# Kernel optimization log

Measured on AMD Instinct MI355X. Metric: run time of the kernel, lower is better.

## Reference

```python
import jax, jax.numpy as jnp
import numpy as np

N = 100000   # nodes
E = 1600000  # edges (before self-loops)
IN = 128     # in_num
H1, C1 = 8, 8    # gat1: 8 heads x 8 channels -> 64 concat
OUT = 32     # out_num (gat2: 1 head x 32)


def setup_inputs() -> dict:
    key = jax.random.key(0)
    ks = jax.random.split(key, 10)
    g = lambda k, shape, fan: (jax.random.normal(k, shape, jnp.float32) / np.sqrt(fan).astype(np.float32))
    return {
        "x": jax.random.normal(ks[0], (N, IN), jnp.float32),
        "edge_index": jax.random.randint(ks[1], (2, E), 0, N, dtype=jnp.int64),
        "W1": g(ks[2], (IN, H1 * C1), IN),
        "a_src1": g(ks[3], (H1, C1), C1),
        "a_dst1": g(ks[4], (H1, C1), C1),
        "b1": jnp.zeros((H1 * C1,), jnp.float32),
        "W2": g(ks[5], (H1 * C1, OUT), H1 * C1),
        "a_src2": g(ks[6], (1, OUT), OUT),
        "a_dst2": g(ks[7], (1, OUT), OUT),
        "b2": jnp.zeros((OUT,), jnp.float32),
    }


def _gat_layer(x, src, dst, W, a_src, a_dst, b, heads, ch):
    # PyG GATConv (concat=True, negative_slope=0.2). Dropout (p=0.6) is a
    # no-op in eval mode and omitted.
    n = x.shape[0]
    h = (x @ W).reshape(n, heads, ch)                        # [N,H,C]
    al_s = jnp.einsum('nhc,hc->nh', h, a_src)                # [N,H]
    al_d = jnp.einsum('nhc,hc->nh', h, a_dst)
    e = jax.nn.leaky_relu(al_s[src] + al_d[dst], negative_slope=0.2)  # [E,H]
    # segment softmax over incoming edges of each dst node
    m = jax.lax.stop_gradient(jax.ops.segment_max(e, dst, num_segments=n))
    ex = jnp.exp(e - m[dst])
    denom = jax.ops.segment_sum(ex, dst, num_segments=n)
    alpha = ex / denom[dst]                                  # [E,H]
    out = jax.ops.segment_sum(h[src] * alpha[:, :, None], dst, num_segments=n)
    return out.reshape(n, heads * ch) + b


def reference(x, edge_index, W1, a_src1, a_dst1, b1, W2, a_src2, a_dst2, b2):
    loop = jnp.arange(N, dtype=edge_index.dtype)
    src = jnp.concatenate([edge_index[0], loop])  # add_self_loops=True (PyG default)
    dst = jnp.concatenate([edge_index[1], loop])
    h = _gat_layer(x, src, dst, W1, a_src1, a_dst1, b1, H1, C1)   # [N,64]
    out = _gat_layer(h, src, dst, W2, a_src2, a_dst2, b2, 1, OUT)  # [N,OUT]
    return out
```

## Files before the change

kernel.cpp:

```cpp
#include <hip/hip_runtime.h>
#include <hip/hip_bf16.h>


#define SLAB  4096
#define STG   8192
#define NBUCK 512

typedef float v2f __attribute__((ext_vector_type(2)));

__device__ __forceinline__ float lrelu02(float x) { return x > 0.f ? x : 0.2f * x; }

__device__ __forceinline__ unsigned short f2bf(float v) {
    __hip_bfloat16 b = __float2bfloat16(v);
    return __builtin_bit_cast(unsigned short, b);
}

__device__ __forceinline__ void accum8(uint4 hv, float ex, v2f* acc) {
    v2f ex2 = {ex, ex};
#pragma unroll
    for (int q = 0; q < 4; ++q) {
        unsigned u = (&hv.x)[q];
        v2f h2 = {__uint_as_float(u << 16), __uint_as_float(u & 0xffff0000u)};
        acc[q] = __builtin_elementwise_fma(h2, ex2, acc[q]);
    }
}

__device__ __forceinline__ v2f shfl_xor_v2(v2f v, int mask) {
    v2f r;
    r.x = __shfl_xor(v.x, mask, 64);
    r.y = __shfl_xor(v.y, mask, 64);
    return r;
}

__device__ __forceinline__ void scatter_body(char* smem, int vbid,
                                             const int* __restrict__ ei,
                                             int e_real, int e_total, unsigned M,
                                             int* __restrict__ bcur_pad,
                                             unsigned* __restrict__ pairs) {
    int* cnt   = (int*)smem;
    int* loff  = cnt + 512;
    int* lcur  = loff + 512;
    int* gbase = lcur + 512;
    int* sw    = gbase + 512;

    const int t = threadIdx.x;
    const int base = vbid * STG;
    cnt[t] = 0; cnt[t + 256] = 0;
    __syncthreads();

    int rs[STG / 256], rd[STG / 256], rb[STG / 256];
#pragma unroll
    for (int k = 0; k < STG / 256; ++k) {
        int i = base + k * 256 + t;
        bool val = i < e_total;
        int s = 0, d = 0;
        if (val) {
            if (i < e_real) { s = ei[i]; d = ei[e_real + i]; }
            else            { s = d = i - e_real; }
        }
        int b = val ? (int)__umulhi((unsigned)d, M) : -1;
        rs[k] = s; rd[k] = d; rb[k] = b;
        if (val) atomicAdd(&cnt[b], 1);
    }
    __syncthreads();

    loff[t] = cnt[t]; loff[t + 256] = cnt[t + 256];
    __syncthreads();
    for (int off = 1; off < 512; off <<= 1) {
        int v0 = (t >= off) ? loff[t - off] : 0;
        int v1 = (t + 256 >= off) ? loff[t + 256 - off] : 0;
        __syncthreads();
        loff[t] += v0; loff[t + 256] += v1;
        __syncthreads();
    }
    int e0 = loff[t] - cnt[t];
    int e1 = loff[t + 256] - cnt[t + 256];
    loff[t] = e0;           loff[t + 256] = e1;
    lcur[t] = e0;           lcur[t + 256] = e1;
    gbase[t]       = t * SLAB         + atomicAdd(&bcur_pad[t * 16], cnt[t]);
    gbase[t + 256] = (t + 256) * SLAB + atomicAdd(&bcur_pad[(t + 256) * 16],
                                                  cnt[t + 256]);
    {
        const unsigned long long Mll = M;
        cnt[t]       = (int)((((unsigned long long)t << 32) + Mll - 1) / Mll);
        cnt[t + 256] = (int)((((unsigned long long)(t + 256) << 32) + Mll - 1) / Mll);
    }
    __syncthreads();

#pragma unroll
    for (int k = 0; k < STG / 256; ++k) {
        if (rb[k] >= 0) {
            int lp = atomicAdd(&lcur[rb[k]], 1);
            sw[lp] = rs[k] | ((rd[k] - cnt[rb[k]]) << 17);
        }
    }
    __syncthreads();

#pragma unroll
    for (int q = 0; q < 2; ++q) {
        int b  = t + q * 256;
        int s0 = loff[b];
        int cb = lcur[b] - s0;
        int g  = gbase[b];
        for (int j = 0; j < cb; ++j)
            pairs[g + j] = (unsigned)sw[s0 + j];
    }
}

template<int K, int OUTC, int H, int C, int NPT, int KCHUNK>
__device__ __forceinline__ void gemm_al_body(char* smem, int vbid,
                                             const float* __restrict__ x,
                                             const float* __restrict__ W,
                                             const float* __restrict__ a_src,
                                             const float* __restrict__ a_dst,
                                             unsigned short* __restrict__ h,
                                             float* __restrict__ al_s,
                                             float* __restrict__ al_d,
                                             int n) {
    constexpr int COLG = OUTC / 4;
    constexpr int NG   = 256 / COLG;
    static_assert(NG * 8 == NPT, "tile mismatch");
    constexpr int LDX  = KCHUNK + 1;
    float* Xs = (float*)smem;
    float* Ws = Xs + NPT * LDX;

    const int t    = threadIdx.x;
    const int mg   = t / COLG;
    const int cg   = t % COLG;
    const int base = vbid * NPT;

    float acc[8][4];
#pragma unroll
    for (int i = 0; i < 8; ++i)
#pragma unroll
        for (int j = 0; j < 4; ++j) acc[i][j] = 0.f;

    for (int kc = 0; kc < K; kc += KCHUNK) {
        __syncthreads();
        constexpr int F4R = KCHUNK / 4;
        constexpr int TOTF4 = NPT * F4R;
#pragma unroll
        for (int r = 0; r < TOTF4 / 256; ++r) {
            int f4   = r * 256 + t;
            int node = f4 / F4R;
            int kq   = f4 % F4R;
            int gn   = base + node; if (gn > n - 1) gn = n - 1;
            const float4 v = *(const float4*)&x[(size_t)gn * K + kc + kq * 4];
            float* d = &Xs[node * LDX + kq * 4];
            d[0] = v.x; d[1] = v.y; d[2] = v.z; d[3] = v.w;
        }
        constexpr int WF4 = KCHUNK * OUTC / 4;
        for (int idx = t; idx < WF4; idx += 256)
            *(float4*)&Ws[idx * 4] = *(const float4*)&W[(size_t)kc * OUTC + idx * 4];
        __syncthreads();

#pragma unroll 4
        for (int k = 0; k < KCHUNK; ++k) {
            float4 b = *(const float4*)&Ws[k * OUTC + cg * 4];
            float a[8];
#pragma unroll
            for (int i = 0; i < 8; ++i) a[i] = Xs[(mg * 8 + i) * LDX + k];
#pragma unroll
            for (int i = 0; i < 8; ++i) {
                acc[i][0] += a[i] * b.x;
                acc[i][1] += a[i] * b.y;
                acc[i][2] += a[i] * b.z;
                acc[i][3] += a[i] * b.w;
            }
        }
    }

    const float4 as4 = *(const float4*)&a_src[cg * 4];
    const float4 ad4 = *(const float4*)&a_dst[cg * 4];
    constexpr int GPH = C / 4;
    const int head = cg / GPH;
#pragma unroll
    for (int i = 0; i < 8; ++i) {
        int gn = base + mg * 8 + i;
        bool ok = gn < n;
        if (ok) {
            ushort4 hv;
            hv.x = f2bf(acc[i][0]); hv.y = f2bf(acc[i][1]);
            hv.z = f2bf(acc[i][2]); hv.w = f2bf(acc[i][3]);
            *(ushort4*)&h[(size_t)gn * OUTC + cg * 4] = hv;
        }
        float ps = acc[i][0] * as4.x + acc[i][1] * as4.y +
                   acc[i][2] * as4.z + acc[i][3] * as4.w;
        float pd = acc[i][0] * ad4.x + acc[i][1] * ad4.y +
                   acc[i][2] * ad4.z + acc[i][3] * ad4.w;
#pragma unroll
        for (int s = 1; s < GPH; s <<= 1) {
            ps += __shfl_xor(ps, s, 64);
            pd += __shfl_xor(pd, s, 64);
        }
        if (ok && (cg % GPH) == 0) {
            al_s[(size_t)gn * H + head] = ps;
            al_d[(size_t)gn * H + head] = pd;
        }
    }
}

__global__ __launch_bounds__(256)
void scatter_gemm_kernel(const int* __restrict__ ei, int e_real, int e_total,
                         unsigned M, int* __restrict__ bcur_pad,
                         unsigned* __restrict__ pairs, int ns,
                         const float* __restrict__ x,
                         const float* __restrict__ W1,
                         const float* __restrict__ as1,
                         const float* __restrict__ ad1,
                         unsigned short* __restrict__ h,
                         float* __restrict__ al_s,
                         float* __restrict__ al_d, int n) {
    __shared__ __align__(16) char smem[40960];
    if ((int)blockIdx.x < ns)
        scatter_body(smem, blockIdx.x, ei, e_real, e_total, M, bcur_pad, pairs);
    else
        gemm_al_body<128, 64, 8, 8, 128, 32>(smem, blockIdx.x - ns,
                                             x, W1, as1, ad1, h, al_s, al_d, n);
}

template<int K, int OUTC, int H, int C, int NPT, int KCHUNK>
__global__ __launch_bounds__(256)
void gemm_al_kernel(const float* __restrict__ x, const float* __restrict__ W,
                    const float* __restrict__ a_src, const float* __restrict__ a_dst,
                    unsigned short* __restrict__ h, float* __restrict__ al_s,
                    float* __restrict__ al_d, int n) {
    __shared__ __align__(16) char smem[(NPT * (KCHUNK + 1) + KCHUNK * OUTC) * 4];
    gemm_al_body<K, OUTC, H, C, NPT, KCHUNK>(smem, blockIdx.x, x, W, a_src,
                                             a_dst, h, al_s, al_d, n);
}

__global__ __launch_bounds__(256)
void csr_finalize_kernel(const unsigned* __restrict__ pairs,
                         const int* __restrict__ bcur_pad,
                         unsigned M, int n,
                         int* __restrict__ offsets,
                         int* __restrict__ srcs) {
    const int b = blockIdx.x;
    const int t = threadIdx.x;
    const unsigned long long Mll = M;
    int lo = (int)((((unsigned long long)b << 32) + Mll - 1) / Mll);
    int hi = (int)((((unsigned long long)(b + 1) << 32) + Mll - 1) / Mll);
    if (lo > n) lo = n;
    if (hi > n) hi = n;
    const int R    = hi - lo;
    const int cntb = bcur_pad[b * 16];
    const unsigned* sp = pairs + (size_t)b * SLAB;

    __shared__ int bs[NBUCK];
    __shared__ int ebeg_s;
    bs[t] = bcur_pad[t * 16];
    bs[t + 256] = bcur_pad[(t + 256) * 16];
    __syncthreads();
    for (int off = 1; off < NBUCK; off <<= 1) {
        int v0 = (t >= off) ? bs[t - off] : 0;
        int v1 = (t + 256 >= off) ? bs[t + 256 - off] : 0;
        __syncthreads();
        bs[t] += v0; bs[t + 256] += v1;
        __syncthreads();
    }
    if (t == 0) ebeg_s = (b == 0) ? 0 : bs[b - 1];
    if (b == NBUCK - 1 && t == 0) offsets[n] = bs[NBUCK - 1];
    __syncthreads();
    const int ebeg = ebeg_s;

    __shared__ int deg[256], sc[256], cur[256];
    deg[t] = 0;
    __syncthreads();
    for (int j = t; j < cntb; j += 256)
        atomicAdd(&deg[sp[j] >> 17], 1);
    __syncthreads();

    sc[t] = deg[t];
    __syncthreads();
    for (int off = 1; off < 256; off <<= 1) {
        int v = (t >= off) ? sc[t - off] : 0;
        __syncthreads();
        sc[t] += v;
        __syncthreads();
    }
    int e0 = sc[t] - deg[t];
    cur[t] = e0;
    if (t < R) offsets[lo + t] = ebeg + e0;
    __syncthreads();

    for (int j = t; j < cntb; j += 256) {
        unsigned w = sp[j];
        int pos = atomicAdd(&cur[w >> 17], 1);
        srcs[ebeg + pos] = (int)(w & 0x1FFFFu);
    }
}

template<int H, int C>
__global__ __launch_bounds__(256)
void gat_agg_kernel(const int* __restrict__ offsets,
                    const int* __restrict__ srcs,
                    const float* __restrict__ al_s,
                    const float* __restrict__ al_d,
                    const unsigned short* __restrict__ hfeat,
                    const float* __restrict__ bias,
                    float* __restrict__ out, int n) {
    constexpr int OUTC = H * C;
    constexpr int CG   = OUTC / 8;
    constexpr int ES   = 64 / CG;
    const int wid  = (int)((blockIdx.x * blockDim.x + threadIdx.x) >> 6);
    const int lane = threadIdx.x & 63;
    const int cg   = lane % CG;
    const int es   = lane / CG;
    if (wid >= n) return;
    const int head = (cg * 8) / C;

    const float aldv = al_d[(size_t)wid * H + head];
    const int beg = offsets[wid];
    const int end = offsets[wid + 1];
    const int deg = end - beg;

    v2f acc[4];
#pragma unroll
    for (int q = 0; q < 4; ++q) acc[q] = (v2f){0.f, 0.f};
    float dsum = 0.f;

    if (deg <= ES) {
        int j = beg + es;
        bool v = j < end;
        int s = __builtin_nontemporal_load(&srcs[v ? j : beg]);
        const uint4 hv = *(const uint4*)&hfeat[(size_t)s * OUTC + cg * 8];
        float ls = al_s[(size_t)s * H + head];
        float ex = v ? __expf(lrelu02(ls + aldv)) : 0.f;
        accum8(hv, ex, acc);
        dsum += ex;
    } else if (deg <= 2 * ES) {
        int sA = __builtin_nontemporal_load(&srcs[beg + es]);
        int jB = beg + ES + es;
        bool vB = jB < end;
        int sB = __builtin_nontemporal_load(&srcs[vB ? jB : beg]);
        const uint4 hvA = *(const uint4*)&hfeat[(size_t)sA * OUTC + cg * 8];
        const uint4 hvB = *(const uint4*)&hfeat[(size_t)sB * OUTC + cg * 8];
        float lsA = al_s[(size_t)sA * H + head];
        float lsB = al_s[(size_t)sB * H + head];
        float exA = __expf(lrelu02(lsA + aldv));
        float exB = vB ? __expf(lrelu02(lsB + aldv)) : 0.f;
        accum8(hvA, exA, acc);
        accum8(hvB, exB, acc);
        dsum += exA + exB;
    } else if (deg <= 4 * ES) {
        int sA = __builtin_nontemporal_load(&srcs[beg + es]);
        int sB = __builtin_nontemporal_load(&srcs[beg + ES + es]);
        int jC = beg + 2 * ES + es;
        int jD = beg + 3 * ES + es;
        bool vC = jC < end;
        bool vD = jD < end;
        int sC = __builtin_nontemporal_load(&srcs[vC ? jC : beg]);
        int sD = __builtin_nontemporal_load(&srcs[vD ? jD : beg]);
        const uint4 hvA = *(const uint4*)&hfeat[(size_t)sA * OUTC + cg * 8];
        const uint4 hvB = *(const uint4*)&hfeat[(size_t)sB * OUTC + cg * 8];
        const uint4 hvC = *(const uint4*)&hfeat[(size_t)sC * OUTC + cg * 8];
        const uint4 hvD = *(const uint4*)&hfeat[(size_t)sD * OUTC + cg * 8];
        float lsA = al_s[(size_t)sA * H + head];
        float lsB = al_s[(size_t)sB * H + head];
        float lsC = al_s[(size_t)sC * H + head];
        float lsD = al_s[(size_t)sD * H + head];
        float exA = __expf(lrelu02(lsA + aldv));
        float exB = __expf(lrelu02(lsB + aldv));
        float exC = vC ? __expf(lrelu02(lsC + aldv)) : 0.f;
        float exD = vD ? __expf(lrelu02(lsD + aldv)) : 0.f;
        accum8(hvA, exA, acc);
        accum8(hvB, exB, acc);
        accum8(hvC, exC, acc);
        accum8(hvD, exD, acc);
        dsum += (exA + exB) + (exC + exD);
    } else {
        for (int j0 = beg; j0 < end; j0 += 2 * ES) {
            int jA = j0 + es;
            int jB = j0 + ES + es;
            bool vA = jA < end;
            bool vB = jB < end;
            int sA = __builtin_nontemporal_load(&srcs[vA ? jA : beg]);
            int sB = __builtin_nontemporal_load(&srcs[vB ? jB : beg]);
            const uint4 hvA = *(const uint4*)&hfeat[(size_t)sA * OUTC + cg * 8];
            const uint4 hvB = *(const uint4*)&hfeat[(size_t)sB * OUTC + cg * 8];
            float lsA = al_s[(size_t)sA * H + head];
            float lsB = al_s[(size_t)sB * H + head];
            float exA = vA ? __expf(lrelu02(lsA + aldv)) : 0.f;
            float exB = vB ? __expf(lrelu02(lsB + aldv)) : 0.f;
            accum8(hvA, exA, acc);
            accum8(hvB, exB, acc);
            dsum += exA + exB;
        }
    }

#pragma unroll
    for (int sh = CG; sh < 64; sh <<= 1) {
        dsum += __shfl_xor(dsum, sh, 64);
#pragma unroll
        for (int q = 0; q < 4; ++q) acc[q] += shfl_xor_v2(acc[q], sh);
    }

    if (es == 0) {
        float inv = 1.f / dsum;
        const float4 b0 = *(const float4*)&bias[cg * 8];
        const float4 b1v = *(const float4*)&bias[cg * 8 + 4];
        float4 o0, o1;
        o0.x = acc[0].x * inv + b0.x;
        o0.y = acc[0].y * inv + b0.y;
        o0.z = acc[1].x * inv + b0.z;
        o0.w = acc[1].y * inv + b0.w;
        o1.x = acc[2].x * inv + b1v.x;
        o1.y = acc[2].y * inv + b1v.y;
        o1.z = acc[3].x * inv + b1v.z;
        o1.w = acc[3].y * inv + b1v.w;
        *(float4*)&out[(size_t)wid * OUTC + cg * 8]     = o0;
        *(float4*)&out[(size_t)wid * OUTC + cg * 8 + 4] = o1;
    }
}


extern "C" void kernel_launch(void* const* d_in, const int* in_sizes, int n_in,
                              void* d_out, int out_size, void* d_ws, size_t ws_size,
                              hipStream_t stream) {
    const float* x   = (const float*)d_in[0];
    const int*   ei  = (const int*)  d_in[1];
    const float* W1  = (const float*)d_in[2];
    const float* as1 = (const float*)d_in[3];
    const float* ad1 = (const float*)d_in[4];
    const float* b1  = (const float*)d_in[5];
    const float* W2  = (const float*)d_in[6];
    const float* as2 = (const float*)d_in[7];
    const float* ad2 = (const float*)d_in[8];
    const float* b2  = (const float*)d_in[9];
    float* out = (float*)d_out;

    const int n       = in_sizes[0] / 128;
    const int e_real  = in_sizes[1] / 2;
    const int e_total = e_real + n;
    const unsigned M512 = (unsigned)(((unsigned long long)NBUCK << 32) / (unsigned)n);

    unsigned short* h1u = (unsigned short*)d_ws;
    float* fws  = (float*)d_ws;
    float* als1 = fws  + (size_t)n * 32;
    float* ald1 = als1 + (size_t)n * 8;
    float* agg1 = ald1 + (size_t)n * 8;
    unsigned* pairs = (unsigned*)agg1;
    int* offsets  = (int*)(agg1 + (size_t)n * 64);
    int* srcs     = offsets + (n + 1);
    int* bcur_pad = srcs + e_total;

    const int ns = (e_total + STG - 1) / STG;
    const int g1 = (n + 127) / 128;

    hipMemsetAsync(bcur_pad, 0, NBUCK * 16 * sizeof(int), stream);
    scatter_gemm_kernel<<<ns + g1, 256, 0, stream>>>(
        ei, e_real, e_total, M512, bcur_pad, pairs, ns,
        x, W1, as1, ad1, h1u, als1, ald1, n);
    csr_finalize_kernel<<<NBUCK, 256, 0, stream>>>(pairs, bcur_pad, M512, n,
                                                   offsets, srcs);

    gat_agg_kernel<8, 8><<<(n + 3) / 4, 256, 0, stream>>>(
        offsets, srcs, als1, ald1, h1u, b1, agg1, n);

    gemm_al_kernel<64, 32, 1, 32, 256, 32><<<(n + 255) / 256, 256, 0, stream>>>(
        agg1, W2, as2, ad2, h1u, als1, ald1, n);
    gat_agg_kernel<1, 32><<<(n + 3) / 4, 256, 0, stream>>>(
        offsets, srcs, als1, ald1, h1u, b2, out, n);
}
```

Baseline: 263.3 us.

## Fuse layer-1 aggregation with layer-2 GEMM and attention logits

Layer-1 GAT aggregation and the layer-2 linear projection plus attention-logit computation now run in one kernel. Each wave aggregates NPW nodes and projects the 64-wide result through W2, which is held transposed in shared memory. It then writes bf16 h2 and the two attention logits directly. This removes the fp32 agg1 round trip through global memory and one kernel launch, at the cost of shuffle reductions and a W2 load in every block.

Measured after the change: 283.0 us. 1.07x slower.

```diff
diff --git a/kernel.cpp b/kernel.cpp
--- a/kernel.cpp
+++ b/kernel.cpp
@@ -5,6 +5,7 @@
 #define SLAB  4096
 #define STG   8192
 #define NBUCK 512
+#define NPW   4
 
 typedef float v2f __attribute__((ext_vector_type(2)));
 
@@ -219,17 +220,6 @@
                                              x, W1, as1, ad1, h, al_s, al_d, n);
 }
 
-template<int K, int OUTC, int H, int C, int NPT, int KCHUNK>
-__global__ __launch_bounds__(256)
-void gemm_al_kernel(const float* __restrict__ x, const float* __restrict__ W,
-                    const float* __restrict__ a_src, const float* __restrict__ a_dst,
-                    unsigned short* __restrict__ h, float* __restrict__ al_s,
-                    float* __restrict__ al_d, int n) {
-    __shared__ __align__(16) char smem[(NPT * (KCHUNK + 1) + KCHUNK * OUTC) * 4];
-    gemm_al_body<K, OUTC, H, C, NPT, KCHUNK>(smem, blockIdx.x, x, W, a_src,
-                                             a_dst, h, al_s, al_d, n);
-}
-
 __global__ __launch_bounds__(256)
 void csr_finalize_kernel(const unsigned* __restrict__ pairs,
                          const int* __restrict__ bcur_pad,
@@ -288,6 +278,184 @@
         unsigned w = sp[j];
         int pos = atomicAdd(&cur[w >> 17], 1);
         srcs[ebeg + pos] = (int)(w & 0x1FFFFu);
+    }
+}
+
+__global__ __launch_bounds__(256)
+void gat_agg_fuse_kernel(const int* __restrict__ offsets,
+                         const int* __restrict__ srcs,
+                         const float* __restrict__ al_s,
+                         const float* __restrict__ al_d,
+                         const unsigned short* __restrict__ hfeat,
+                         const float* __restrict__ b1,
+                         const float* __restrict__ W2,
+                         const float* __restrict__ as2,
+                         const float* __restrict__ ad2,
+                         unsigned short* __restrict__ h2,
+                         float* __restrict__ als2,
+                         float* __restrict__ ald2,
+                         int n) {
+    constexpr int H = 8, C = 8, OUTC = 64;
+    constexpr int CG = 8, ES = 8;
+    __shared__ __align__(16) float w2t[32 * 65];
+    __shared__ __align__(16) float a2s[64];
+
+    const int t = threadIdx.x;
+    for (int idx = t; idx < 2048; idx += 256) {
+        int ch = idx >> 5, col = idx & 31;
+        w2t[col * 65 + ch] = W2[idx];
+    }
+    if (t < 32) { a2s[t] = as2[t]; a2s[32 + t] = ad2[t]; }
+    __syncthreads();
+
+    const int lane = t & 63;
+    const int cg   = lane & 7;
+    const int es   = lane >> 3;
+    const int head = cg;
+    const int wv   = (int)((blockIdx.x * blockDim.x + threadIdx.x) >> 6);
+
+    float b1r[8];
+    {
+        const float4 bb0 = *(const float4*)&b1[cg * 8];
+        const float4 bb1 = *(const float4*)&b1[cg * 8 + 4];
+        b1r[0] = bb0.x; b1r[1] = bb0.y; b1r[2] = bb0.z; b1r[3] = bb0.w;
+        b1r[4] = bb1.x; b1r[5] = bb1.y; b1r[6] = bb1.z; b1r[7] = bb1.w;
+    }
+
+    for (int nd = 0; nd < NPW; ++nd) {
+        const int wid = wv * NPW + nd;
+        if (wid >= n) return;
+
+        const float aldv = al_d[(size_t)wid * H + head];
+        const int beg = offsets[wid];
+        const int end = offsets[wid + 1];
+        const int deg = end - beg;
+
+        v2f acc[4];
+#pragma unroll
+        for (int q = 0; q < 4; ++q) acc[q] = (v2f){0.f, 0.f};
+        float dsum = 0.f;
+
+        if (deg <= ES) {
+            int j = beg + es;
+            bool v = j < end;
+            int s = __builtin_nontemporal_load(&srcs[v ? j : beg]);
+            const uint4 hv = *(const uint4*)&hfeat[(size_t)s * OUTC + cg * 8];
+            float ls = al_s[(size_t)s * H + head];
+            float ex = v ? __expf(lrelu02(ls + aldv)) : 0.f;
+            accum8(hv, ex, acc);
+            dsum += ex;
+        } else if (deg <= 2 * ES) {
+            int sA = __builtin_nontemporal_load(&srcs[beg + es]);
+            int jB = beg + ES + es;
+            bool vB = jB < end;
+            int sB = __builtin_nontemporal_load(&srcs[vB ? jB : beg]);
+            const uint4 hvA = *(const uint4*)&hfeat[(size_t)sA * OUTC + cg * 8];
+            const uint4 hvB = *(const uint4*)&hfeat[(size_t)sB * OUTC + cg * 8];
+            float lsA = al_s[(size_t)sA * H + head];
+            float lsB = al_s[(size_t)sB * H + head];
+            float exA = __expf(lrelu02(lsA + aldv));
+            float exB = vB ? __expf(lrelu02(lsB + aldv)) : 0.f;
+            accum8(hvA, exA, acc);
+            accum8(hvB, exB, acc);
+            dsum += exA + exB;
+        } else if (deg <= 4 * ES) {
+            int sA = __builtin_nontemporal_load(&srcs[beg + es]);
+            int sB = __builtin_nontemporal_load(&srcs[beg + ES + es]);
+            int jC = beg + 2 * ES + es;
+            int jD = beg + 3 * ES + es;
+            bool vC = jC < end;
+            bool vD = jD < end;
+            int sC = __builtin_nontemporal_load(&srcs[vC ? jC : beg]);
+            int sD = __builtin_nontemporal_load(&srcs[vD ? jD : beg]);
+            const uint4 hvA = *(const uint4*)&hfeat[(size_t)sA * OUTC + cg * 8];
+            const uint4 hvB = *(const uint4*)&hfeat[(size_t)sB * OUTC + cg * 8];
+            const uint4 hvC = *(const uint4*)&hfeat[(size_t)sC * OUTC + cg * 8];
+            const uint4 hvD = *(const uint4*)&hfeat[(size_t)sD * OUTC + cg * 8];
+            float lsA = al_s[(size_t)sA * H + head];
+            float lsB = al_s[(size_t)sB * H + head];
+            float lsC = al_s[(size_t)sC * H + head];
+            float lsD = al_s[(size_t)sD * H + head];
+            float exA = __expf(lrelu02(lsA + aldv));
+            float exB = __expf(lrelu02(lsB + aldv));
+            float exC = vC ? __expf(lrelu02(lsC + aldv)) : 0.f;
+            float exD = vD ? __expf(lrelu02(lsD + aldv)) : 0.f;
+            accum8(hvA, exA, acc);
+            accum8(hvB, exB, acc);
+            accum8(hvC, exC, acc);
+            accum8(hvD, exD, acc);
+            dsum += (exA + exB) + (exC + exD);
+        } else {
+            for (int j0 = beg; j0 < end; j0 += 2 * ES) {
+                int jA = j0 + es;
+                int jB = j0 + ES + es;
+                bool vA = jA < end;
+                bool vB = jB < end;
+                int sA = __builtin_nontemporal_load(&srcs[vA ? jA : beg]);
+                int sB = __builtin_nontemporal_load(&srcs[vB ? jB : beg]);
+                const uint4 hvA = *(const uint4*)&hfeat[(size_t)sA * OUTC + cg * 8];
+                const uint4 hvB = *(const uint4*)&hfeat[(size_t)sB * OUTC + cg * 8];
+                float lsA = al_s[(size_t)sA * H + head];
+                float lsB = al_s[(size_t)sB * H + head];
+                float exA = vA ? __expf(lrelu02(lsA + aldv)) : 0.f;
+                float exB = vB ? __expf(lrelu02(lsB + aldv)) : 0.f;
+                accum8(hvA, exA, acc);
+                accum8(hvB, exB, acc);
+                dsum += exA + exB;
+            }
+        }
+
+#pragma unroll
+        for (int sh = CG; sh < 64; sh <<= 1) {
+            dsum += __shfl_xor(dsum, sh, 64);
+#pragma unroll
+            for (int q = 0; q < 4; ++q) acc[q] += shfl_xor_v2(acc[q], sh);
+        }
+
+        const float inv = 1.f / dsum;
+        float r8[8];
+#pragma unroll
+        for (int q = 0; q < 4; ++q) {
+            r8[2 * q]     = acc[q].x * inv + b1r[2 * q];
+            r8[2 * q + 1] = acc[q].y * inv + b1r[2 * q + 1];
+        }
+        float p0 = 0.f, p1 = 0.f, p2 = 0.f, p3 = 0.f;
+        {
+            const float* w0 = &w2t[(4 * es + 0) * 65 + 8 * cg];
+            const float* w1 = &w2t[(4 * es + 1) * 65 + 8 * cg];
+            const float* w2 = &w2t[(4 * es + 2) * 65 + 8 * cg];
+            const float* w3 = &w2t[(4 * es + 3) * 65 + 8 * cg];
+#pragma unroll
+            for (int j = 0; j < 8; ++j) {
+                p0 += r8[j] * w0[j];
+                p1 += r8[j] * w1[j];
+                p2 += r8[j] * w2[j];
+                p3 += r8[j] * w3[j];
+            }
+        }
+#pragma unroll
+        for (int m = 1; m < 8; m <<= 1) {
+            p0 += __shfl_xor(p0, m, 64);
+            p1 += __shfl_xor(p1, m, 64);
+            p2 += __shfl_xor(p2, m, 64);
+            p3 += __shfl_xor(p3, m, 64);
+        }
+        if (cg == 0) {
+            ushort4 hv;
+            hv.x = f2bf(p0); hv.y = f2bf(p1);
+            hv.z = f2bf(p2); hv.w = f2bf(p3);
+            *(ushort4*)&h2[(size_t)wid * 32 + es * 4] = hv;
+        }
+        const float4 a4 = *(const float4*)&a2s[4 * es];
+        const float4 d4 = *(const float4*)&a2s[32 + 4 * es];
+        float ps = p0 * a4.x + p1 * a4.y + p2 * a4.z + p3 * a4.w;
+        float pd = p0 * d4.x + p1 * d4.y + p2 * d4.z + p3 * d4.w;
+#pragma unroll
+        for (int m = 8; m < 64; m <<= 1) {
+            ps += __shfl_xor(ps, m, 64);
+            pd += __shfl_xor(pd, m, 64);
+        }
+        if (lane == 0) { als2[wid] = ps; ald2[wid] = pd; }
     }
 }
 
@@ -439,9 +607,12 @@
     float* fws  = (float*)d_ws;
     float* als1 = fws  + (size_t)n * 32;
     float* ald1 = als1 + (size_t)n * 8;
-    float* agg1 = ald1 + (size_t)n * 8;
-    unsigned* pairs = (unsigned*)agg1;
-    int* offsets  = (int*)(agg1 + (size_t)n * 64);
+    float* reg2 = ald1 + (size_t)n * 8;
+    unsigned* pairs = (unsigned*)reg2;
+    unsigned short* h2 = (unsigned short*)reg2;
+    float* als2 = (float*)(h2 + (size_t)n * 32);
+    float* ald2 = als2 + n;
+    int* offsets  = (int*)(reg2 + (size_t)n * 64);
     int* srcs     = offsets + (n + 1);
     int* bcur_pad = srcs + e_total;
 
@@ -455,11 +626,10 @@
     csr_finalize_kernel<<<NBUCK, 256, 0, stream>>>(pairs, bcur_pad, M512, n,
                                                    offsets, srcs);
 
-    gat_agg_kernel<8, 8><<<(n + 3) / 4, 256, 0, stream>>>(
-        offsets, srcs, als1, ald1, h1u, b1, agg1, n);
-
-    gemm_al_kernel<64, 32, 1, 32, 256, 32><<<(n + 255) / 256, 256, 0, stream>>>(
-        agg1, W2, as2, ad2, h1u, als1, ald1, n);
+    const int nwaves = (n + NPW - 1) / NPW;
+    gat_agg_fuse_kernel<<<(nwaves + 3) / 4, 256, 0, stream>>>(
+        offsets, srcs, als1, ald1, h1u, b1, W2, as2, ad2, h2, als2, ald2, n);
+
     gat_agg_kernel<1, 32><<<(n + 3) / 4, 256, 0, stream>>>(
-        offsets, srcs, als1, ald1, h1u, b2, out, n);
-}
+        offsets, srcs, als2, ald2, h2, b2, out, n);
+}
```

## Split layer-1 GEMM blocks between scatter and CSR-finalize kernels

Applied to the files above, without the earlier changes.

The layer-1 GEMM work is now split across two launches. The first GSPLIT tiles run alongside the edge scatter as before, and the remaining tiles are co-scheduled with the CSR finalize blocks in a new fused csr_gemm kernel. The aim is to balance work so the 512-block CSR finalize, which is short on parallelism, shares the GPU with GEMM tiles instead of running alone. This adds a hardcoded split point that depends on n, and if n shrinks below GSPLIT*128 the grid size math (g1 - GSPLIT) could go negative.

Result: faster. 256.7 us (-2.5%).

```diff
diff --git a/kernel.cpp b/kernel.cpp
--- a/kernel.cpp
+++ b/kernel.cpp
@@ -5,6 +5,7 @@
 #define SLAB  4096
 #define STG   8192
 #define NBUCK 512
+#define GSPLIT 300
 
 typedef float v2f __attribute__((ext_vector_type(2)));
 
@@ -197,6 +198,69 @@
             al_s[(size_t)gn * H + head] = ps;
             al_d[(size_t)gn * H + head] = pd;
         }
+    }
+}
+
+__device__ __forceinline__ void csr_body(char* smem, int b,
+                                         const unsigned* __restrict__ pairs,
+                                         const int* __restrict__ bcur_pad,
+                                         unsigned M, int n,
+                                         int* __restrict__ offsets,
+                                         int* __restrict__ srcs) {
+    int* bs  = (int*)smem;
+    int* deg = bs + 512;
+    int* sc  = deg + 256;
+    int* cur = sc + 256;
+    int* ebeg_p = cur + 256;
+
+    const int t = threadIdx.x;
+    const unsigned long long Mll = M;
+    int lo = (int)((((unsigned long long)b << 32) + Mll - 1) / Mll);
+    int hi = (int)((((unsigned long long)(b + 1) << 32) + Mll - 1) / Mll);
+    if (lo > n) lo = n;
+    if (hi > n) hi = n;
+    const int R    = hi - lo;
+    const int cntb = bcur_pad[b * 16];
+    const unsigned* sp = pairs + (size_t)b * SLAB;
+
+    bs[t] = bcur_pad[t * 16];
+    bs[t + 256] = bcur_pad[(t + 256) * 16];
+    __syncthreads();
+    for (int off = 1; off < NBUCK; off <<= 1) {
+        int v0 = (t >= off) ? bs[t - off] : 0;
+        int v1 = (t + 256 >= off) ? bs[t + 256 - off] : 0;
+        __syncthreads();
+        bs[t] += v0; bs[t + 256] += v1;
+        __syncthreads();
+    }
+    if (t == 0) *ebeg_p = (b == 0) ? 0 : bs[b - 1];
+    if (b == NBUCK - 1 && t == 0) offsets[n] = bs[NBUCK - 1];
+    __syncthreads();
+    const int ebeg = *ebeg_p;
+
+    deg[t] = 0;
+    __syncthreads();
+    for (int j = t; j < cntb; j += 256)
+        atomicAdd(&deg[sp[j] >> 17], 1);
+    __syncthreads();
+
+    sc[t] = deg[t];
+    __syncthreads();
+    for (int off = 1; off < 256; off <<= 1) {
+        int v = (t >= off) ? sc[t - off] : 0;
+        __syncthreads();
+        sc[t] += v;
+        __syncthreads();
+    }
+    int e0 = sc[t] - deg[t];
+    cur[t] = e0;
+    if (t < R) offsets[lo + t] = ebeg + e0;
+    __syncthreads();
+
+    for (int j = t; j < cntb; j += 256) {
+        unsigned w = sp[j];
+        int pos = atomicAdd(&cur[w >> 17], 1);
+        srcs[ebeg + pos] = (int)(w & 0x1FFFFu);
     }
 }
 
@@ -219,6 +283,28 @@
                                              x, W1, as1, ad1, h, al_s, al_d, n);
 }
 
+__global__ __launch_bounds__(256)
+void csr_gemm_kernel(const unsigned* __restrict__ pairs,
+                     const int* __restrict__ bcur_pad,
+                     unsigned M,
+                     int* __restrict__ offsets,
+                     int* __restrict__ srcs,
+                     const float* __restrict__ x,
+                     const float* __restrict__ W1,
+                     const float* __restrict__ as1,
+                     const float* __restrict__ ad1,
+                     unsigned short* __restrict__ h,
+                     float* __restrict__ al_s,
+                     float* __restrict__ al_d, int n) {
+    __shared__ __align__(16) char smem[25088];
+    if ((int)blockIdx.x < NBUCK)
+        csr_body(smem, blockIdx.x, pairs, bcur_pad, M, n, offsets, srcs);
+    else
+        gemm_al_body<128, 64, 8, 8, 128, 32>(smem,
+                                             GSPLIT + ((int)blockIdx.x - NBUCK),
+                                             x, W1, as1, ad1, h, al_s, al_d, n);
+}
+
 template<int K, int OUTC, int H, int C, int NPT, int KCHUNK>
 __global__ __launch_bounds__(256)
 void gemm_al_kernel(const float* __restrict__ x, const float* __restrict__ W,
@@ -228,67 +314,6 @@
     __shared__ __align__(16) char smem[(NPT * (KCHUNK + 1) + KCHUNK * OUTC) * 4];
     gemm_al_body<K, OUTC, H, C, NPT, KCHUNK>(smem, blockIdx.x, x, W, a_src,
                                              a_dst, h, al_s, al_d, n);
-}
-
-__global__ __launch_bounds__(256)
-void csr_finalize_kernel(const unsigned* __restrict__ pairs,
-                         const int* __restrict__ bcur_pad,
-                         unsigned M, int n,
-                         int* __restrict__ offsets,
-                         int* __restrict__ srcs) {
-    const int b = blockIdx.x;
-    const int t = threadIdx.x;
-    const unsigned long long Mll = M;
-    int lo = (int)((((unsigned long long)b << 32) + Mll - 1) / Mll);
-    int hi = (int)((((unsigned long long)(b + 1) << 32) + Mll - 1) / Mll);
-    if (lo > n) lo = n;
-    if (hi > n) hi = n;
-    const int R    = hi - lo;
-    const int cntb = bcur_pad[b * 16];
-    const unsigned* sp = pairs + (size_t)b * SLAB;
-
-    __shared__ int bs[NBUCK];
-    __shared__ int ebeg_s;
-    bs[t] = bcur_pad[t * 16];
-    bs[t + 256] = bcur_pad[(t + 256) * 16];
-    __syncthreads();
-    for (int off = 1; off < NBUCK; off <<= 1) {
-        int v0 = (t >= off) ? bs[t - off] : 0;
-        int v1 = (t + 256 >= off) ? bs[t + 256 - off] : 0;
-        __syncthreads();
-        bs[t] += v0; bs[t + 256] += v1;
-        __syncthreads();
-    }
-    if (t == 0) ebeg_s = (b == 0) ? 0 : bs[b - 1];
-    if (b == NBUCK - 1 && t == 0) offsets[n] = bs[NBUCK - 1];
-    __syncthreads();
-    const int ebeg = ebeg_s;
-
-    __shared__ int deg[256], sc[256], cur[256];
-    deg[t] = 0;
-    __syncthreads();
-    for (int j = t; j < cntb; j += 256)
-        atomicAdd(&deg[sp[j] >> 17], 1);
-    __syncthreads();
-
-    sc[t] = deg[t];
-    __syncthreads();
-    for (int off = 1; off < 256; off <<= 1) {
-        int v = (t >= off) ? sc[t - off] : 0;
-        __syncthreads();
-        sc[t] += v;
-        __syncthreads();
-    }
-    int e0 = sc[t] - deg[t];
-    cur[t] = e0;
-    if (t < R) offsets[lo + t] = ebeg + e0;
-    __syncthreads();
-
-    for (int j = t; j < cntb; j += 256) {
-        unsigned w = sp[j];
-        int pos = atomicAdd(&cur[w >> 17], 1);
-        srcs[ebeg + pos] = (int)(w & 0x1FFFFu);
-    }
 }
 
 template<int H, int C>
@@ -449,11 +474,13 @@
     const int g1 = (n + 127) / 128;
 
     hipMemsetAsync(bcur_pad, 0, NBUCK * 16 * sizeof(int), stream);
-    scatter_gemm_kernel<<<ns + g1, 256, 0, stream>>>(
+    scatter_gemm_kernel<<<ns + GSPLIT, 256, 0, stream>>>(
         ei, e_real, e_total, M512, bcur_pad, pairs, ns,
         x, W1, as1, ad1, h1u, als1, ald1, n);
-    csr_finalize_kernel<<<NBUCK, 256, 0, stream>>>(pairs, bcur_pad, M512, n,
-                                                   offsets, srcs);
+
+    csr_gemm_kernel<<<NBUCK + (g1 - GSPLIT), 256, 0, stream>>>(
+        pairs, bcur_pad, M512, offsets, srcs,
+        x, W1, as1, ad1, h1u, als1, ald1, n);
 
     gat_agg_kernel<8, 8><<<(n + 3) / 4, 256, 0, stream>>>(
         offsets, srcs, als1, ald1, h1u, b1, agg1, n);
```
